# Optimization experiments

Hardware: AMD Instinct MI355X
Metric: run time of the kernel (lower is better)

Reference implementation:

```python
import jax, jax.numpy as jnp
import numpy as np

E = 100000   # number of directed edges
T = 500000   # number of triplets
H = 128      # hidden_channels
INT = 64     # int_emb_size
NR = 6       # num_radial
NS = 7       # num_spherical
BD = BA = BT = 8  # basis emb sizes
NB = 1       # num_before_skip
NA = 2       # num_after_skip


def setup_inputs() -> dict:
    key = jax.random.key(0)
    ks = jax.random.split(key, 32)
    def rn(k, shape, fan_in):
        return jax.random.normal(k, shape, dtype=jnp.float32) / np.float32(np.sqrt(fan_in))
    inp = {}
    inp["x1"] = jax.random.normal(ks[0], (E, H), dtype=jnp.float32)
    inp["rbf0"] = jax.random.normal(ks[1], (E, NR), dtype=jnp.float32)
    inp["sbf"] = jax.random.normal(ks[2], (T, NS * NR), dtype=jnp.float32)
    inp["t"] = jax.random.normal(ks[3], (T, NS * NS * NR), dtype=jnp.float32)
    inp["q_r"] = jax.random.normal(ks[4], (E, 1), dtype=jnp.float32)
    inp["W_rbf1"] = rn(ks[5], (NR, BD), NR)
    inp["W_rbf2"] = rn(ks[6], (BD, H), BD)
    inp["W_sbf1"] = rn(ks[7], (NS * NR, BA), NS * NR)
    inp["W_sbf2"] = rn(ks[8], (BA, INT), BA)
    inp["W_t1"] = rn(ks[9], (NS * NS * NR, BT), NS * NS * NR)
    inp["W_t2"] = rn(ks[10], (BT, INT), BT)
    inp["W_rbf"] = rn(ks[11], (NR, H), NR)
    inp["W_kj"] = rn(ks[12], (H, H), H)
    inp["b_kj"] = jnp.zeros((H,), jnp.float32)
    inp["W_ji"] = rn(ks[13], (H, H), H)
    inp["b_ji"] = jnp.zeros((H,), jnp.float32)
    inp["W_down"] = rn(ks[14], (H, INT), H)
    inp["W_up"] = rn(ks[15], (INT, H), INT)
    inp["W_lin"] = rn(ks[16], (H, H), H)
    inp["b_lin"] = jnp.zeros((H,), jnp.float32)
    inp["resb_W1"] = rn(ks[17], (NB, H, H), H)
    inp["resb_b1"] = jnp.zeros((NB, H), jnp.float32)
    inp["resb_W2"] = rn(ks[18], (NB, H, H), H)
    inp["resb_b2"] = jnp.zeros((NB, H), jnp.float32)
    inp["resa_W1"] = rn(ks[19], (NA, H, H), H)
    inp["resa_b1"] = jnp.zeros((NA, H), jnp.float32)
    inp["resa_W2"] = rn(ks[20], (NA, H, H), H)
    inp["resa_b2"] = jnp.zeros((NA, H), jnp.float32)
    inp["idx_kj"] = jax.random.randint(ks[21], (T,), 0, E)
    inp["idx_ji"] = jax.random.randint(ks[22], (T,), 0, E)
    return inp


def reference(x1, rbf0, sbf, t, q_r,
              W_rbf1, W_rbf2, W_sbf1, W_sbf2, W_t1, W_t2, W_rbf,
              W_kj, b_kj, W_ji, b_ji, W_down, W_up, W_lin, b_lin,
              resb_W1, resb_b1, resb_W2, resb_b2,
              resa_W1, resa_b1, resa_W2, resa_b2,
              idx_kj, idx_ji):
    act = jax.nn.selu

    def res_block(x, W1, b1, W2, b2):
        return x + act(act(x @ W1 + b1) @ W2 + b2)

    x_ji = act(x1 @ W_ji + b_ji)                      # [E, H]
    x_kj = act(x1 @ W_kj + b_kj)                      # [E, H]

    rbf = (rbf0 @ W_rbf1) @ W_rbf2                    # [E, H]
    x_kj = x_kj * rbf
    x_kj = act(x_kj @ W_down)                         # [E, INT]

    sbf_p = (sbf @ W_sbf1) @ W_sbf2                   # [T, INT]
    x_kj = x_kj[idx_kj] * sbf_p                       # gather -> [T, INT]

    t_p = (t @ W_t1) @ W_t2                           # [T, INT]
    x_kj = x_kj * t_p

    x_kj = jax.ops.segment_sum(x_kj, idx_ji, num_segments=x1.shape[0])  # [E, INT]
    x_kj = act(x_kj @ W_up)                           # [E, H]

    e1 = x_ji + x_kj
    for i in range(resb_W1.shape[0]):
        e1 = res_block(e1, resb_W1[i], resb_b1[i], resb_W2[i], resb_b2[i])
    e1 = act(e1 @ W_lin + b_lin) + x1
    for i in range(resa_W1.shape[0]):
        e1 = res_block(e1, resa_W1[i], resa_b1[i], resa_W2[i], resa_b2[i])

    e2 = (rbf0 @ W_rbf) * e1
    return (e1, e2)
```

## Files before the change

kernel.cpp:

```cpp
#include <hip/hip_runtime.h>
#include <hip/hip_bf16.h>

#define EDGES 100000
#define TRIPS 500000
#define HC 128
#define IC 64
#define NRC 6
#define SBF_K 42
#define T_K 294
#define T_KSTEPS 10
#define S_KSTEPS 2

typedef __attribute__((ext_vector_type(8))) short bf16x8;
typedef __attribute__((ext_vector_type(4))) float f32x4;
typedef __attribute__((ext_vector_type(2))) float f32x2;

__device__ __forceinline__ float selu_f(float x) {
    const float scale = 1.0507009873554805f;
    const float alpha = 1.6732632423543772f;
    return x > 0.f ? scale * x : scale * alpha * expm1f(x);
}

__device__ __forceinline__ unsigned short f2bf(float f) {
    unsigned int u = __float_as_uint(f);
    u += 0x7fffu + ((u >> 16) & 1u);
    return (unsigned short)(u >> 16);
}

__device__ __forceinline__ unsigned cvtpk(float a, float b) {
    unsigned o;
    asm("v_cvt_pk_bf16_f32 %0, %1, %2" : "=v"(o) : "v"(a), "v"(b));
    return o;
}

__device__ __forceinline__ void gl_lds16(const char* g, char* l) {
    __builtin_amdgcn_global_load_lds(
        (const __attribute__((address_space(1))) void*)g,
        (__attribute__((address_space(3))) void*)l, 16, 0, 0);
}

__device__ __forceinline__ bf16x8 ldsA(const unsigned short* act, int row, int kbf) {
    int byte = row * 256 + kbf * 2;
    byte ^= (row & 7) << 4;
    return *(const bf16x8*)((const char*)act + byte);
}
__device__ __forceinline__ void ldsW(unsigned short* act, int row, int col, unsigned short v) {
    int byte = row * 256 + col * 2;
    byte ^= (row & 7) << 4;
    *(unsigned short*)((char*)act + byte) = v;
}
__device__ __forceinline__ void ldsW8B(unsigned short* act, int row, int col4,
                                       float a, float b, float c, float d) {
    unsigned long long v = (unsigned long long)(f2bf(a) | ((unsigned)f2bf(b) << 16)) |
                           ((unsigned long long)(f2bf(c) | ((unsigned)f2bf(d) << 16)) << 32);
    int byte = row * 256 + col4 * 8;
    byte ^= (row & 7) << 4;
    *(unsigned long long*)((char*)act + byte) = v;
}

template <int KS>
__device__ __forceinline__ void mm2(const unsigned short* act, const bf16x8* B,
                                    int lane, f32x4* acc) {
    const int ar = lane & 15;
    const int koff = (lane >> 4) * 8;
#pragma unroll
    for (int mt = 0; mt < 2; mt++) {
        f32x4 c = {0.f, 0.f, 0.f, 0.f};
#pragma unroll
        for (int ks = 0; ks < KS; ks++) {
            bf16x8 a = ldsA(act, mt * 16 + ar, ks * 32 + koff);
            c = __builtin_amdgcn_mfma_f32_16x16x32_bf16(a, B[ks], c, 0, 0, 0);
        }
        acc[mt] = c;
    }
}

__device__ __forceinline__ void pack_w(const float* __restrict__ W, int K, int N,
                                       unsigned short* __restrict__ dst, int tid, int stride) {
    const int nt = N >> 4;
    const int total = (K >> 5) * nt * 512;
    for (int idx = tid; idx < total; idx += stride) {
        int j = idx & 7, l = (idx >> 3) & 63;
        int t = idx >> 9;
        int n = t % nt, ks = t / nt;
        int k = ks * 32 + ((l >> 4) << 3) + j;
        int c = n * 16 + (l & 15);
        dst[idx] = f2bf(W[k * N + c]);
    }
}

__global__ void combos_kernel(const float* __restrict__ W_rbf1, const float* __restrict__ W_rbf2,
                              const float* __restrict__ W_sbf1, const float* __restrict__ W_sbf2,
                              const float* __restrict__ W_t1,   const float* __restrict__ W_t2,
                              const float* __restrict__ W_ji,   const float* __restrict__ W_kj,
                              const float* __restrict__ W_down, const float* __restrict__ W_up,
                              const float* __restrict__ resbW1, const float* __restrict__ resbW2,
                              const float* __restrict__ W_lin,
                              const float* __restrict__ resaW1, const float* __restrict__ resaW2,
                              float* __restrict__ Wrbf_c,
                              unsigned short* __restrict__ Wt_pack,
                              unsigned short* __restrict__ Ws_pack,
                              unsigned short* __restrict__ Pji, unsigned short* __restrict__ Pkj,
                              unsigned short* __restrict__ Pdown, unsigned short* __restrict__ Pup,
                              unsigned short* __restrict__ Prb1, unsigned short* __restrict__ Prb2,
                              unsigned short* __restrict__ Plin,
                              unsigned short* __restrict__ Pra10, unsigned short* __restrict__ Pra20,
                              unsigned short* __restrict__ Pra11, unsigned short* __restrict__ Pra21) {
    int tid = blockIdx.x * blockDim.x + threadIdx.x;
    int stride = gridDim.x * blockDim.x;
    for (int idx = tid; idx < NRC * HC; idx += stride) {
        int r = idx / HC, h = idx % HC;
        float s = 0.f;
        for (int b = 0; b < 8; b++) s += W_rbf1[r * 8 + b] * W_rbf2[b * HC + h];
        Wrbf_c[idx] = s;
    }
    for (int idx = tid; idx < T_KSTEPS * 4 * 64 * 8; idx += stride) {
        int j = idx & 7, l = (idx >> 3) & 63, n = (idx >> 9) & 3, s = idx >> 11;
        int k = s * 32 + (l >> 4) * 8 + j;
        int c = n * 16 + (l & 15);
        float v = 0.f;
        if (k < T_K)
            for (int b = 0; b < 8; b++) v += W_t1[k * 8 + b] * W_t2[b * IC + c];
        Wt_pack[idx] = f2bf(v);
    }
    for (int idx = tid; idx < S_KSTEPS * 4 * 64 * 8; idx += stride) {
        int j = idx & 7, l = (idx >> 3) & 63, n = (idx >> 9) & 3, s = idx >> 11;
        int k = s * 32 + (l >> 4) * 8 + j;
        int c = n * 16 + (l & 15);
        float v = 0.f;
        if (k < SBF_K)
            for (int b = 0; b < 8; b++) v += W_sbf1[k * 8 + b] * W_sbf2[b * IC + c];
        Ws_pack[idx] = f2bf(v);
    }
    pack_w(W_ji,   HC, HC, Pji,   tid, stride);
    pack_w(W_kj,   HC, HC, Pkj,   tid, stride);
    pack_w(W_down, HC, IC, Pdown, tid, stride);
    pack_w(W_up,   IC, HC, Pup,   tid, stride);
    pack_w(resbW1, HC, HC, Prb1,  tid, stride);
    pack_w(resbW2, HC, HC, Prb2,  tid, stride);
    pack_w(W_lin,  HC, HC, Plin,  tid, stride);
    pack_w(resaW1,           HC, HC, Pra10, tid, stride);
    pack_w(resaW2,           HC, HC, Pra20, tid, stride);
    pack_w(resaW1 + HC * HC, HC, HC, Pra11, tid, stride);
    pack_w(resaW2 + HC * HC, HC, HC, Pra21, tid, stride);
}

__global__ __launch_bounds__(512) void edge_front_mfma(
    const float* __restrict__ x1, const float* __restrict__ rbf0,
    const unsigned short* __restrict__ Pji, const unsigned short* __restrict__ Pkj,
    const unsigned short* __restrict__ Pdown,
    const float* __restrict__ bji, const float* __restrict__ bkj,
    const float* __restrict__ Wrbf_c,
    float* __restrict__ xji_out, float* __restrict__ xkjd_out,
    float* __restrict__ seg) {
    __shared__ __align__(16) unsigned short act[32 * 128];
    __shared__ float rbfs[32][8];
    const int tid = threadIdx.x;
    const int lane = tid & 63;
    const int w = tid >> 6;
    const int e0 = blockIdx.x * 32;

    ((float4*)(seg + (size_t)e0 * IC))[tid] = float4{0.f, 0.f, 0.f, 0.f};

    bf16x8 Bji[4], Bkj[4];
#pragma unroll
    for (int ks = 0; ks < 4; ks++) {
        Bji[ks] = *(const bf16x8*)(Pji + (size_t)((ks * 8 + w) * 64 + lane) * 8);
        Bkj[ks] = *(const bf16x8*)(Pkj + (size_t)((ks * 8 + w) * 64 + lane) * 8);
    }
    const int ntd = w & 3, mtd = w >> 2;
    bf16x8 Bd[4];
#pragma unroll
    for (int ks = 0; ks < 4; ks++)
        Bd[ks] = *(const bf16x8*)(Pdown + (size_t)((ks * 4 + ntd) * 64 + lane) * 8);

    {
        const float4* s4 = (const float4*)(x1 + (size_t)e0 * HC);
#pragma unroll
        for (int i = tid; i < 1024; i += 512) {
            float4 v = s4[i];
            ldsW8B(act, i >> 5, i & 31, v.x, v.y, v.z, v.w);
        }
        if (tid < 192) rbfs[tid / 6][tid % 6] = rbf0[(size_t)e0 * NRC + tid];
    }
    __syncthreads();

    const int ar = lane & 15;
    const int koff = (lane >> 4) * 8;
    f32x4 aj[2], ak[2];
#pragma unroll
    for (int mt = 0; mt < 2; mt++) {
        f32x4 cj = {0.f, 0.f, 0.f, 0.f};
        f32x4 ck = {0.f, 0.f, 0.f, 0.f};
#pragma unroll
        for (int ks = 0; ks < 4; ks++) {
            bf16x8 a = ldsA(act, mt * 16 + ar, ks * 32 + koff);
            cj = __builtin_amdgcn_mfma_f32_16x16x32_bf16(a, Bji[ks], cj, 0, 0, 0);
            ck = __builtin_amdgcn_mfma_f32_16x16x32_bf16(a, Bkj[ks], ck, 0, 0, 0);
        }
        aj[mt] = cj; ak[mt] = ck;
    }
    __syncthreads();

    const int ch = w * 16 + (lane & 15);
    const int rg = (lane >> 4) * 4;
    {
        float bjv = bji[ch], bkv = bkj[ch];
        float wr[6];
#pragma unroll
        for (int q = 0; q < 6; q++) wr[q] = Wrbf_c[q * HC + ch];
#pragma unroll
        for (int mt = 0; mt < 2; mt++) {
#pragma unroll
            for (int r = 0; r < 4; r++) {
                int m = mt * 16 + rg + r;
                float rv = 0.f;
#pragma unroll
                for (int q = 0; q < 6; q++) rv += rbfs[m][q] * wr[q];
                xji_out[(size_t)(e0 + m) * HC + ch] = selu_f(aj[mt][r] + bjv);
                float xk = selu_f(ak[mt][r] + bkv) * rv;
                ldsW(act, m, ch, f2bf(xk));
            }
        }
    }
    __syncthreads();

    f32x4 cd = {0.f, 0.f, 0.f, 0.f};
#pragma unroll
    for (int ks = 0; ks < 4; ks++) {
        bf16x8 a = ldsA(act, mtd * 16 + ar, ks * 32 + koff);
        cd = __builtin_amdgcn_mfma_f32_16x16x32_bf16(a, Bd[ks], cd, 0, 0, 0);
    }
    const int chd = ntd * 16 + (lane & 15);
#pragma unroll
    for (int r = 0; r < 4; r++)
        xkjd_out[(size_t)(e0 + mtd * 16 + rg + r) * IC + chd] = selu_f(cd[r]);
}

#define T2_IMG_B 18816
#define S2_IMG_B 2688
#define LDS2_TOT (T2_IMG_B + S2_IMG_B + 64 + 64 + 64)
__global__ __launch_bounds__(256) void triplet_mfma8(
    const float* __restrict__ sbf, const float* __restrict__ tmat,
    const unsigned short* __restrict__ Wt_pack,
    const unsigned short* __restrict__ Ws_pack,
    const float* __restrict__ xkjd,
    const int* __restrict__ idx_kj, const int* __restrict__ idx_ji,
    float* __restrict__ seg, int nslab) {
    __shared__ __align__(16) char lds[LDS2_TOT];
    char* t_img = lds;
    char* s_img = lds + T2_IMG_B;
    int* kj_s = (int*)(lds + T2_IMG_B + S2_IMG_B + 64);
    int* ji_s = kj_s + 16;
    const int tid = threadIdx.x;
    const int lane = tid & 63;
    const int w = tid >> 6;
    const int lr = lane & 15;
    const int lq = lane >> 4;
    const int ch = w * 16 + lr;

    bf16x8 bt_w[T_KSTEPS], bs_w[S_KSTEPS];
#pragma unroll
    for (int s = 0; s < T_KSTEPS; s++)
        bt_w[s] = *(const bf16x8*)(Wt_pack + (size_t)((s * 4 + w) * 64 + lane) * 8);
#pragma unroll
    for (int s = 0; s < S_KSTEPS; s++)
        bs_w[s] = *(const bf16x8*)(Ws_pack + (size_t)((s * 4 + w) * 64 + lane) * 8);

    for (int slab = blockIdx.x; slab < nslab; slab += gridDim.x) {
        const size_t t0 = (size_t)slab * 16;
        const char* tsrc = (const char*)tmat + (size_t)slab * T2_IMG_B;
        const char* ssrc = (const char*)sbf + (size_t)slab * S2_IMG_B;

        for (int i = w; i < 22; i += 4) {
            if (i < 19) {
                int off = i * 1024 + lane * 16;
                if (off < T2_IMG_B) gl_lds16(tsrc + off, t_img + off);
            } else {
                int off = (i - 19) * 1024 + lane * 16;
                if (off < S2_IMG_B) gl_lds16(ssrc + off, s_img + off);
            }
        }
        if (tid < 16) { kj_s[tid] = idx_kj[t0 + tid]; ji_s[tid] = idx_ji[t0 + tid]; }
        __syncthreads();

        f32x4 acc_t = {0.f, 0.f, 0.f, 0.f};
        f32x4 acc_s = {0.f, 0.f, 0.f, 0.f};
        {
            const char* tp = t_img + lr * 1176 + lq * 32;
#pragma unroll
            for (int ks = 0; ks < T_KSTEPS; ks++) {
                f32x2 p0 = *(const f32x2*)(tp + ks * 128);
                f32x2 p1 = *(const f32x2*)(tp + ks * 128 + 8);
                f32x2 p2 = *(const f32x2*)(tp + ks * 128 + 16);
                f32x2 p3 = *(const f32x2*)(tp + ks * 128 + 24);
                union { unsigned u[4]; bf16x8 v; } a;
                a.u[0] = cvtpk(p0.x, p0.y); a.u[1] = cvtpk(p1.x, p1.y);
                a.u[2] = cvtpk(p2.x, p2.y); a.u[3] = cvtpk(p3.x, p3.y);
                acc_t = __builtin_amdgcn_mfma_f32_16x16x32_bf16(a.v, bt_w[ks], acc_t, 0, 0, 0);
            }
            const char* sp = s_img + lr * 168 + lq * 32;
#pragma unroll
            for (int ks = 0; ks < S_KSTEPS; ks++) {
                f32x2 p0 = *(const f32x2*)(sp + ks * 128);
                f32x2 p1 = *(const f32x2*)(sp + ks * 128 + 8);
                f32x2 p2 = *(const f32x2*)(sp + ks * 128 + 16);
                f32x2 p3 = *(const f32x2*)(sp + ks * 128 + 24);
                union { unsigned u[4]; bf16x8 v; } a;
                a.u[0] = cvtpk(p0.x, p0.y); a.u[1] = cvtpk(p1.x, p1.y);
                a.u[2] = cvtpk(p2.x, p2.y); a.u[3] = cvtpk(p3.x, p3.y);
                acc_s = __builtin_amdgcn_mfma_f32_16x16x32_bf16(a.v, bs_w[ks], acc_s, 0, 0, 0);
            }
        }

#pragma unroll
        for (int r = 0; r < 4; r++) {
            int ml = lq * 4 + r;
            float y = xkjd[(size_t)kj_s[ml] * IC + ch] * acc_s[r] * acc_t[r];
            atomicAdd(&seg[(size_t)ji_s[ml] * IC + ch], y);
        }
        __syncthreads();
    }
}

__global__ __launch_bounds__(512, 4) void edge_back_mfma(
    const float* __restrict__ seg, const float* __restrict__ xji,
    const float* __restrict__ x1, const float* __restrict__ rbf0,
    const unsigned short* __restrict__ Pup,
    const unsigned short* __restrict__ Prb1, const unsigned short* __restrict__ Prb2,
    const unsigned short* __restrict__ Plin,
    const unsigned short* __restrict__ Pra10, const unsigned short* __restrict__ Pra20,
    const unsigned short* __restrict__ Pra11, const unsigned short* __restrict__ Pra21,
    const float* __restrict__ bb1, const float* __restrict__ bb2,
    const float* __restrict__ blin,
    const float* __restrict__ ba1, const float* __restrict__ ba2,
    const float* __restrict__ Wrbf,
    float* __restrict__ e1_out, float* __restrict__ e2_out) {
    __shared__ __align__(16) unsigned short act[32 * 128];
    __shared__ float rbfs[32][8];
    const int tid = threadIdx.x;
    const int lane = tid & 63;
    const int w = tid >> 6;
    const int e0 = blockIdx.x * 32;
    const int ch = w * 16 + (lane & 15);
    const int rg = (lane >> 4) * 4;

    bf16x8 BA[4], BB[4];
#define LOADW(DST, P, N)                                                        \
    _Pragma("unroll")                                                           \
    for (int ks = 0; ks < N; ks++)                                              \
        DST[ks] = *(const bf16x8*)((P) + (size_t)((ks * 8 + w) * 64 + lane) * 8);

    LOADW(BA, Pup, 2)

    {
        const float4* s4 = (const float4*)(seg + (size_t)e0 * IC);
        float4 v = s4[tid];
        ldsW8B(act, tid >> 4, tid & 15, v.x, v.y, v.z, v.w);
        if (tid < 192) rbfs[tid / 6][tid % 6] = rbf0[(size_t)e0 * NRC + tid];
    }
    float skip[2][4], x1v[2][4];
#pragma unroll
    for (int mt = 0; mt < 2; mt++)
#pragma unroll
        for (int r = 0; r < 4; r++) {
            skip[mt][r] = xji[(size_t)(e0 + mt * 16 + rg + r) * HC + ch];
            x1v[mt][r]  = x1 [(size_t)(e0 + mt * 16 + rg + r) * HC + ch];
        }
    __syncthreads();

    f32x4 acc[2];
    float h[2][4];

    mm2<2>(act, BA, lane, acc);
    LOADW(BB, Prb1, 4)
    __syncthreads();
#pragma unroll
    for (int mt = 0; mt < 2; mt++)
#pragma unroll
        for (int r = 0; r < 4; r++) {
            h[mt][r] = selu_f(acc[mt][r]) + skip[mt][r];
            ldsW(act, mt * 16 + rg + r, ch, f2bf(h[mt][r]));
            skip[mt][r] = h[mt][r];
        }
    __syncthreads();

    mm2<4>(act, BB, lane, acc);
    LOADW(BA, Prb2, 4)
    __syncthreads();
    {
        float bv = bb1[ch];
#pragma unroll
        for (int mt = 0; mt < 2; mt++)
#pragma unroll
            for (int r = 0; r < 4; r++)
                ldsW(act, mt * 16 + rg + r, ch, f2bf(selu_f(acc[mt][r] + bv)));
    }
    __syncthreads();

    mm2<4>(act, BA, lane, acc);
    LOADW(BB, Plin, 4)
    __syncthreads();
    {
        float bv = bb2[ch];
#pragma unroll
        for (int mt = 0; mt < 2; mt++)
#pragma unroll
            for (int r = 0; r < 4; r++) {
                h[mt][r] = skip[mt][r] + selu_f(acc[mt][r] + bv);
                ldsW(act, mt * 16 + rg + r, ch, f2bf(h[mt][r]));
            }
    }
    __syncthreads();

    mm2<4>(act, BB, lane, acc);
    LOADW(BA, Pra10, 4)
    __syncthreads();
    {
        float bv = blin[ch];
#pragma unroll
        for (int mt = 0; mt < 2; mt++)
#pragma unroll
            for (int r = 0; r < 4; r++) {
                h[mt][r] = selu_f(acc[mt][r] + bv) + x1v[mt][r];
                ldsW(act, mt * 16 + rg + r, ch, f2bf(h[mt][r]));
                skip[mt][r] = h[mt][r];
            }
    }
    __syncthreads();

    mm2<4>(act, BA, lane, acc);
    LOADW(BB, Pra20, 4)
    __syncthreads();
    {
        float bv = ba1[ch];
#pragma unroll
        for (int mt = 0; mt < 2; mt++)
#pragma unroll
            for (int r = 0; r < 4; r++)
                ldsW(act, mt * 16 + rg + r, ch, f2bf(selu_f(acc[mt][r] + bv)));
    }
    __syncthreads();

    mm2<4>(act, BB, lane, acc);
    LOADW(BA, Pra11, 4)
    __syncthreads();
    {
        float bv = ba2[ch];
#pragma unroll
        for (int mt = 0; mt < 2; mt++)
#pragma unroll
            for (int r = 0; r < 4; r++) {
                h[mt][r] = skip[mt][r] + selu_f(acc[mt][r] + bv);
                ldsW(act, mt * 16 + rg + r, ch, f2bf(h[mt][r]));
                skip[mt][r] = h[mt][r];
            }
    }
    __syncthreads();

    mm2<4>(act, BA, lane, acc);
    LOADW(BB, Pra21, 4)
    __syncthreads();
    {
        float bv = ba1[HC + ch];
#pragma unroll
        for (int mt = 0; mt < 2; mt++)
#pragma unroll
            for (int r = 0; r < 4; r++)
                ldsW(act, mt * 16 + rg + r, ch, f2bf(selu_f(acc[mt][r] + bv)));
    }
    __syncthreads();

    mm2<4>(act, BB, lane, acc);
    {
        float bv = ba2[HC + ch];
        float wr[6];
#pragma unroll
        for (int q = 0; q < 6; q++) wr[q] = Wrbf[q * HC + ch];
#pragma unroll
        for (int mt = 0; mt < 2; mt++)
#pragma unroll
            for (int r = 0; r < 4; r++) {
                int m = mt * 16 + rg + r;
                float v = skip[mt][r] + selu_f(acc[mt][r] + bv);
                float rv = 0.f;
#pragma unroll
                for (int q = 0; q < 6; q++) rv += rbfs[m][q] * wr[q];
                size_t e = (size_t)(e0 + m);
                e1_out[e * HC + ch] = v;
                e2_out[e * HC + ch] = rv * v;
            }
    }
#undef LOADW
}

extern "C" void kernel_launch(void* const* d_in, const int* in_sizes, int n_in,
                              void* d_out, int out_size, void* d_ws, size_t ws_size,
                              hipStream_t stream) {
    const float* x1     = (const float*)d_in[0];
    const float* rbf0   = (const float*)d_in[1];
    const float* sbf    = (const float*)d_in[2];
    const float* tmat   = (const float*)d_in[3];
    const float* W_rbf1 = (const float*)d_in[5];
    const float* W_rbf2 = (const float*)d_in[6];
    const float* W_sbf1 = (const float*)d_in[7];
    const float* W_sbf2 = (const float*)d_in[8];
    const float* W_t1   = (const float*)d_in[9];
    const float* W_t2   = (const float*)d_in[10];
    const float* W_rbf  = (const float*)d_in[11];
    const float* W_kj   = (const float*)d_in[12];
    const float* b_kj   = (const float*)d_in[13];
    const float* W_ji   = (const float*)d_in[14];
    const float* b_ji   = (const float*)d_in[15];
    const float* W_down = (const float*)d_in[16];
    const float* W_up   = (const float*)d_in[17];
    const float* W_lin  = (const float*)d_in[18];
    const float* b_lin  = (const float*)d_in[19];
    const float* resbW1 = (const float*)d_in[20];
    const float* resbb1 = (const float*)d_in[21];
    const float* resbW2 = (const float*)d_in[22];
    const float* resbb2 = (const float*)d_in[23];
    const float* resaW1 = (const float*)d_in[24];
    const float* resab1 = (const float*)d_in[25];
    const float* resaW2 = (const float*)d_in[26];
    const float* resab2 = (const float*)d_in[27];
    const int* idx_kj   = (const int*)d_in[28];
    const int* idx_ji   = (const int*)d_in[29];

    float* ws = (float*)d_ws;
    float* Wrbf_c = ws;
    unsigned short* u0 = (unsigned short*)(ws + 768);
    unsigned short* Wt_pack = u0;
    unsigned short* Ws_pack = Wt_pack + 20480;
    unsigned short* Pji   = Ws_pack + 4096;
    unsigned short* Pkj   = Pji + 16384;
    unsigned short* Pdown = Pkj + 16384;
    unsigned short* Pup   = Pdown + 8192;
    unsigned short* Prb1  = Pup + 8192;
    unsigned short* Prb2  = Prb1 + 16384;
    unsigned short* Plin  = Prb2 + 16384;
    unsigned short* Pra10 = Plin + 16384;
    unsigned short* Pra20 = Pra10 + 16384;
    unsigned short* Pra11 = Pra20 + 16384;
    unsigned short* Pra21 = Pra11 + 16384;
    float* xkjd = ws + 768 + 94208;
    float* seg  = xkjd + (size_t)EDGES * IC;

    float* e1_out = (float*)d_out;
    float* e2_out = e1_out + (size_t)EDGES * HC;
    float* xji    = e1_out;

    combos_kernel<<<64, 256, 0, stream>>>(W_rbf1, W_rbf2, W_sbf1, W_sbf2, W_t1, W_t2,
                                          W_ji, W_kj, W_down, W_up, resbW1, resbW2,
                                          W_lin, resaW1, resaW2,
                                          Wrbf_c, Wt_pack, Ws_pack,
                                          Pji, Pkj, Pdown, Pup, Prb1, Prb2, Plin,
                                          Pra10, Pra20, Pra11, Pra21);
    edge_front_mfma<<<EDGES / 32, 512, 0, stream>>>(x1, rbf0, Pji, Pkj, Pdown,
                                                    b_ji, b_kj, Wrbf_c, xji, xkjd, seg);
    triplet_mfma8<<<4096, 256, 0, stream>>>(sbf, tmat, Wt_pack, Ws_pack, xkjd,
                                            idx_kj, idx_ji, seg, TRIPS / 16);
    edge_back_mfma<<<EDGES / 32, 512, 0, stream>>>(seg, xji, x1, rbf0,
                                                   Pup, Prb1, Prb2, Plin,
                                                   Pra10, Pra20, Pra11, Pra21,
                                                   resbb1, resbb2, b_lin,
                                                   resab1, resab2, W_rbf,
                                                   e1_out, e2_out);
}
```

Before: 332.4 us.

## Double-buffer triplet slabs in LDS with 8-triplet slabs

The triplet kernel now stages the next slab's t/sbf rows and indices into a second LDS buffer while computing the current one, so global loads overlap with MFMA work. Slabs shrink from 16 to 8 triplets: rows 8-15 of each MFMA tile duplicate rows 0-7 and only half the lanes do the gather and atomic scatter. This halves the per-slab staging footprint, which keeps total LDS about the same despite double buffering. In exchange, half the MFMA throughput is wasted and there are twice as many loop iterations and barriers.

Result: slower. 417.4 us (+25.6%).

```diff
diff --git a/kernel.cpp b/kernel.cpp
--- a/kernel.cpp
+++ b/kernel.cpp
@@ -237,21 +237,18 @@
         xkjd_out[(size_t)(e0 + mtd * 16 + rg + r) * IC + chd] = selu_f(cd[r]);
 }
 
-#define T2_IMG_B 18816
-#define S2_IMG_B 2688
-#define LDS2_TOT (T2_IMG_B + S2_IMG_B + 64 + 64 + 64)
-__global__ __launch_bounds__(256) void triplet_mfma8(
+#define T3_IMG_B 9408
+#define S3_IMG_B 1344
+#define BUF_B (T3_IMG_B + S3_IMG_B)
+__global__ __launch_bounds__(256) void triplet_mfma9(
     const float* __restrict__ sbf, const float* __restrict__ tmat,
     const unsigned short* __restrict__ Wt_pack,
     const unsigned short* __restrict__ Ws_pack,
     const float* __restrict__ xkjd,
     const int* __restrict__ idx_kj, const int* __restrict__ idx_ji,
     float* __restrict__ seg, int nslab) {
-    __shared__ __align__(16) char lds[LDS2_TOT];
-    char* t_img = lds;
-    char* s_img = lds + T2_IMG_B;
-    int* kj_s = (int*)(lds + T2_IMG_B + S2_IMG_B + 64);
-    int* ji_s = kj_s + 16;
+    __shared__ __align__(16) char lds[2 * BUF_B + 128];
+    int* kj0 = (int*)(lds + 2 * BUF_B);
     const int tid = threadIdx.x;
     const int lane = tid & 63;
     const int w = tid >> 6;
@@ -267,27 +264,40 @@
     for (int s = 0; s < S_KSTEPS; s++)
         bs_w[s] = *(const bf16x8*)(Ws_pack + (size_t)((s * 4 + w) * 64 + lane) * 8);
 
-    for (int slab = blockIdx.x; slab < nslab; slab += gridDim.x) {
-        const size_t t0 = (size_t)slab * 16;
-        const char* tsrc = (const char*)tmat + (size_t)slab * T2_IMG_B;
-        const char* ssrc = (const char*)sbf + (size_t)slab * S2_IMG_B;
-
-        for (int i = w; i < 22; i += 4) {
-            if (i < 19) {
-                int off = i * 1024 + lane * 16;
-                if (off < T2_IMG_B) gl_lds16(tsrc + off, t_img + off);
-            } else {
-                int off = (i - 19) * 1024 + lane * 16;
-                if (off < S2_IMG_B) gl_lds16(ssrc + off, s_img + off);
-            }
-        }
-        if (tid < 16) { kj_s[tid] = idx_kj[t0 + tid]; ji_s[tid] = idx_ji[t0 + tid]; }
-        __syncthreads();
+#define STAGE(B, SLAB)                                                             \
+    {                                                                              \
+        const char* tsrc = (const char*)tmat + (size_t)(SLAB) * T3_IMG_B;          \
+        const char* ssrc = (const char*)sbf + (size_t)(SLAB) * S3_IMG_B;           \
+        char* tb = lds + (B) * BUF_B;                                              \
+        char* sb = tb + T3_IMG_B;                                                  \
+        for (int i = w; i < 12; i += 4) {                                          \
+            if (i < 10) {                                                          \
+                int off = i * 1024 + lane * 16;                                    \
+                if (off < T3_IMG_B) gl_lds16(tsrc + off, tb + off);                \
+            } else {                                                               \
+                int off = (i - 10) * 1024 + lane * 16;                             \
+                if (off < S3_IMG_B) gl_lds16(ssrc + off, sb + off);                \
+            }                                                                      \
+        }                                                                          \
+        if (tid < 8) {                                                             \
+            kj0[(B) * 8 + tid]      = idx_kj[(size_t)(SLAB) * 8 + tid];            \
+            kj0[16 + (B) * 8 + tid] = idx_ji[(size_t)(SLAB) * 8 + tid];            \
+        }                                                                          \
+    }
+
+    int slab = blockIdx.x;
+    if (slab < nslab) STAGE(0, slab)
+    __syncthreads();
+
+    int it = 0;
+    for (; slab < nslab; slab += gridDim.x, it ^= 1) {
+        int nxt = slab + gridDim.x;
+        if (nxt < nslab) STAGE(it ^ 1, nxt)
 
         f32x4 acc_t = {0.f, 0.f, 0.f, 0.f};
         f32x4 acc_s = {0.f, 0.f, 0.f, 0.f};
         {
-            const char* tp = t_img + lr * 1176 + lq * 32;
+            const char* tp = lds + it * BUF_B + (lr & 7) * 1176 + lq * 32;
 #pragma unroll
             for (int ks = 0; ks < T_KSTEPS; ks++) {
                 f32x2 p0 = *(const f32x2*)(tp + ks * 128);
@@ -299,7 +309,7 @@
                 a.u[2] = cvtpk(p2.x, p2.y); a.u[3] = cvtpk(p3.x, p3.y);
                 acc_t = __builtin_amdgcn_mfma_f32_16x16x32_bf16(a.v, bt_w[ks], acc_t, 0, 0, 0);
             }
-            const char* sp = s_img + lr * 168 + lq * 32;
+            const char* sp = lds + it * BUF_B + T3_IMG_B + (lr & 7) * 168 + lq * 32;
 #pragma unroll
             for (int ks = 0; ks < S_KSTEPS; ks++) {
                 f32x2 p0 = *(const f32x2*)(sp + ks * 128);
@@ -313,14 +323,17 @@
             }
         }
 
-#pragma unroll
-        for (int r = 0; r < 4; r++) {
-            int ml = lq * 4 + r;
-            float y = xkjd[(size_t)kj_s[ml] * IC + ch] * acc_s[r] * acc_t[r];
-            atomicAdd(&seg[(size_t)ji_s[ml] * IC + ch], y);
+        if (lq < 2) {
+#pragma unroll
+            for (int r = 0; r < 4; r++) {
+                int ml = lq * 4 + r;
+                float y = xkjd[(size_t)kj0[it * 8 + ml] * IC + ch] * acc_s[r] * acc_t[r];
+                atomicAdd(&seg[(size_t)kj0[16 + it * 8 + ml] * IC + ch], y);
+            }
         }
         __syncthreads();
     }
+#undef STAGE
 }
 
 __global__ __launch_bounds__(512, 4) void edge_back_mfma(
@@ -558,8 +571,8 @@
                                           Pra10, Pra20, Pra11, Pra21);
     edge_front_mfma<<<EDGES / 32, 512, 0, stream>>>(x1, rbf0, Pji, Pkj, Pdown,
                                                     b_ji, b_kj, Wrbf_c, xji, xkjd, seg);
-    triplet_mfma8<<<4096, 256, 0, stream>>>(sbf, tmat, Wt_pack, Ws_pack, xkjd,
-                                            idx_kj, idx_ji, seg, TRIPS / 16);
+    triplet_mfma9<<<4096, 256, 0, stream>>>(sbf, tmat, Wt_pack, Ws_pack, xkjd,
+                                            idx_kj, idx_ji, seg, TRIPS / 8);
     edge_back_mfma<<<EDGES / 32, 512, 0, stream>>>(seg, xji, x1, rbf0,
                                                    Pup, Prb1, Prb2, Plin,
                                                    Pra10, Pra20, Pra11, Pra21,
```
